# Performance work log

Measured on AMD Instinct MI355X. Metric: run time of the kernel, lower is better.

Reference implementation:

```python
import jax, jax.numpy as jnp
import numpy as np

B, CIN, COUT = 4, 32, 32
D1, D2, D3 = 64, 64, 64
M1, M2, M3 = 32, 32, 17  # n_modes with last dim -> 32//2+1 after rfft redundancy
INIT_STD = (2.0 / (CIN + COUT)) ** 0.5


def setup_inputs() -> dict:
    key = jax.random.key(0)
    k_x, k_wr, k_wi, k_b = jax.random.split(key, 4)
    x = jax.random.normal(k_x, (B, CIN, D1, D2, D3), dtype=jnp.float32)
    # ComplexDense factorized weight, normal_(0, init_std) on real and imag parts
    w_real = INIT_STD * jax.random.normal(k_wr, (CIN, COUT, M1, M2, M3), dtype=jnp.float32)
    w_imag = INIT_STD * jax.random.normal(k_wi, (CIN, COUT, M1, M2, M3), dtype=jnp.float32)
    # bias: (n_layers=1, out_channels, 1, 1, 1); we take index 0 slice
    bias = INIT_STD * jax.random.normal(k_b, (1, COUT, 1, 1, 1), dtype=jnp.float32)
    return {"x": x, "w_real": w_real, "w_imag": w_imag, "bias": bias}


def reference(x, w_real, w_imag, bias):
    fft_axes = (-3, -2, -1)
    b, cin, d1, d2, d3 = x.shape
    f3 = d3 // 2 + 1
    # forward rFFT, shift all but last (real) axis so low modes are centered
    xf = jnp.fft.rfftn(x, axes=fft_axes)               # (B, Cin, D1, D2, f3) complex
    xf = jnp.fft.fftshift(xf, axes=fft_axes[:-1])
    weight = w_real + 1j * w_imag                       # (Cin, Cout, M1, M2, M3)
    m1, m2, m3 = weight.shape[2:]
    s1, s2 = (d1 - m1) // 2, (d2 - m2) // 2
    xs = xf[:, :, s1:s1 + m1, s2:s2 + m2, :m3]          # centered low modes
    # channel contraction in Fourier space: abcde,bfcde->afcde
    out_modes = jnp.einsum('abcde,bfcde->afcde', xs, weight)
    out_fft = jnp.zeros((b, weight.shape[1], d1, d2, f3), dtype=out_modes.dtype)
    out_fft = out_fft.at[:, :, s1:s1 + m1, s2:s2 + m2, :m3].set(out_modes)
    # torch applies fftshift (not ifftshift); identical for even sizes
    out_fft = jnp.fft.fftshift(out_fft, axes=fft_axes[:-1])
    out = jnp.fft.irfftn(out_fft, s=(d1, d2, d3), axes=fft_axes)
    return out + bias[0]
```

## Files before the change

### kernel.cpp

```cpp
#include <hip/hip_runtime.h>
#include <math.h>

static constexpr int NB  = 4;
static constexpr int NC  = 32;

__device__ __attribute__((aligned(256))) float T3F[64 * 48];
__device__ __attribute__((aligned(256))) float2 T3I2[17 * 64];
__device__ __attribute__((aligned(256))) float T12F[64 * 64];
__device__ __attribute__((aligned(256))) float TINV[32 * 128];

__global__ __launch_bounds__(256) void k0_init() {
    const int t = blockIdx.x * 256 + threadIdx.x;
    if (t < 64 * 17) {
        int n = t / 17, k = t % 17;
        int idx = (n * k) & 63;
        float s, c;
        sincospif(idx / 32.0f, &s, &c);
        T3F[n * 48 + 2 * k] = c;  T3F[n * 48 + 2 * k + 1] = -s;
    }
    if (t < 64) {
        for (int q = 34; q < 48; ++q) T3F[t * 48 + q] = 0.f;
    }
    if (t < 17 * 64) {
        int k = t >> 6, n = t & 63;
        int idx = (n * k) & 63;
        float s, c;
        sincospif(idx / 32.0f, &s, &c);
        T3I2[t] = make_float2(c, s);
    }
    if (t < 64 * 32) {
        int n = t / 32, p = t % 32;
        int o = (p + 48) & 63;
        int idx = (o * n) & 63;
        float s, c;
        sincospif(idx / 32.0f, &s, &c);
        T12F[n * 64 + 2 * p] = c;  T12F[n * 64 + 2 * p + 1] = -s;
    }
    if (t < 32 * 64) {
        int p = t / 64, n = t % 64;
        int o = (p + 48) & 63;
        int idx = (o * n) & 63;
        float s, c;
        sincospif(idx / 32.0f, &s, &c);
        TINV[p * 128 + 2 * n] = c;  TINV[p * 128 + 2 * n + 1] = s;
    }
}

__device__ __forceinline__ void cmadd(float2& a, float2 x, float wx, float wy) {
    a.x = fmaf(x.x, wx, fmaf(-x.y, wy, a.x));
    a.y = fmaf(x.x, wy, fmaf( x.y, wx, a.y));
}

__global__ __launch_bounds__(64)
void k1_rfft_d3(const float* __restrict__ x, float2* __restrict__ o1) {
    __shared__ float tile[64 * 65];
    const int t = threadIdx.x, bid = blockIdx.x;
    const float4* src4 = (const float4*)(x + (size_t)bid * 4096);
    for (int j = 0; j < 16; ++j) {
        int f4 = j * 64 + t;
        float4 v = src4[f4];
        int d2 = f4 >> 4, n0 = (f4 & 15) << 2;
        float* p = &tile[d2 * 65 + n0];
        p[0] = v.x; p[1] = v.y; p[2] = v.z; p[3] = v.w;
    }
    __syncthreads();
    float ar[17], ai[17];
#pragma unroll
    for (int k = 0; k < 17; ++k) { ar[k] = 0.f; ai[k] = 0.f; }
    const float* row = &tile[t * 65];
    for (int n = 0; n < 32; ++n) {
        float xa = row[n], xb = row[n + 32];
        float se = xa + xb, so = xa - xb;
        const float* w = &T3F[n * 48];
#pragma unroll
        for (int k = 0; k < 17; ++k) {
            float xv = (k & 1) ? so : se;
            ar[k] = fmaf(xv, w[2 * k], ar[k]);
            ai[k] = fmaf(xv, w[2 * k + 1], ai[k]);
        }
    }
    const int bc = bid >> 6, d1 = bid & 63;
    float2* dst = o1 + (size_t)bc * (17 * 4096) + d1 * 64 + t;
#pragma unroll
    for (int k = 0; k < 17; ++k)
        dst[(size_t)k * 4096] = make_float2(ar[k], ai[k]);
}

__global__ __launch_bounds__(256)
void k2a_dft_d2(const float2* __restrict__ in, float2* __restrict__ T) {
    __shared__ float smem[8320];
    float* re = smem;
    float* im = smem + 64 * 65;
    const int t = threadIdx.x;
    const size_t base = (size_t)blockIdx.x * 4096;
    for (int j = 0; j < 16; ++j) {
        int idx = j * 256 + t;
        float2 v = in[base + idx];
        int d1 = idx >> 6, n2 = idx & 63;
        re[d1 * 65 + n2] = v.x;
        im[d1 * 65 + n2] = v.y;
    }
    __syncthreads();
    const int d1 = t & 63;
    const int pg = __builtin_amdgcn_readfirstlane(t >> 6);
    float2 acc[8];
#pragma unroll
    for (int j = 0; j < 8; ++j) acc[j] = make_float2(0.f, 0.f);
    const float* rrow = &re[d1 * 65];
    const float* irow = &im[d1 * 65];
#pragma unroll 2
    for (int n2 = 0; n2 < 64; ++n2) {
        float xr = rrow[n2], xi = irow[n2];
        const float* w = &T12F[n2 * 64 + pg * 16];
#pragma unroll
        for (int j = 0; j < 8; ++j)
            cmadd(acc[j], make_float2(xr, xi), w[2 * j], w[2 * j + 1]);
    }
    __syncthreads();
    float2* tile = (float2*)smem;
#pragma unroll
    for (int j = 0; j < 8; ++j) tile[d1 * 33 + pg * 8 + j] = acc[j];
    __syncthreads();
    float2* dst = T + (size_t)blockIdx.x * 2048;
#pragma unroll
    for (int q = 0; q < 8; ++q) {
        int e = t * 8 + q;
        dst[e] = tile[(e >> 5) * 33 + (e & 31)];
    }
}

__global__ __launch_bounds__(544)
void k2b_dft_d1(const float2* __restrict__ T, float2* __restrict__ Y) {
    __shared__ float2 tile[8 * 544];
    const int u = threadIdx.x;
    const int bc = blockIdx.x, pg = blockIdx.y;
    const int k3 = u >> 5, p2 = u & 31;
    const float2* src = T + ((size_t)bc * 17 + k3) * 2048 + p2;
    float2 acc[8];
#pragma unroll
    for (int j = 0; j < 8; ++j) acc[j] = make_float2(0.f, 0.f);
#pragma unroll 2
    for (int n1 = 0; n1 < 64; ++n1) {
        float2 xv = src[n1 * 32];
        const float* w = &T12F[n1 * 64 + pg * 16];
#pragma unroll
        for (int j = 0; j < 8; ++j)
            cmadd(acc[j], xv, w[2 * j], w[2 * j + 1]);
    }
#pragma unroll
    for (int j = 0; j < 8; ++j)
        tile[j * 544 + p2 * 17 + k3] = acc[j];
    __syncthreads();
    float2* dst = Y + (size_t)bc * 17408 + (size_t)pg * 8 * 544;
#pragma unroll
    for (int i = 0; i < 8; ++i)
        dst[u + i * 544] = tile[u + i * 544];
}

__global__ __launch_bounds__(64)
void k3_mix(const float2* __restrict__ Y, const float* __restrict__ wr,
            const float* __restrict__ wi, float2* __restrict__ Z) {
    const int m = blockIdx.x * 64 + threadIdx.x;
    const int ch = blockIdx.y;
    float2 acc[4][2];
#pragma unroll
    for (int a = 0; a < 4; ++a)
#pragma unroll
        for (int co = 0; co < 2; ++co) acc[a][co] = make_float2(0.f, 0.f);
#pragma unroll 8
    for (int cin = 0; cin < 32; ++cin) {
        float2 xv[4];
#pragma unroll
        for (int a = 0; a < 4; ++a)
            xv[a] = Y[((size_t)a * 32 + cin) * 17408 + m];
        size_t wb = ((size_t)cin * 32 + ch * 2) * 17408 + m;
#pragma unroll
        for (int co = 0; co < 2; ++co) {
            float wrv = wr[wb + (size_t)co * 17408];
            float wiv = wi[wb + (size_t)co * 17408];
#pragma unroll
            for (int a = 0; a < 4; ++a)
                cmadd(acc[a][co], xv[a], wrv, wiv);
        }
    }
#pragma unroll
    for (int a = 0; a < 4; ++a)
#pragma unroll
        for (int co = 0; co < 2; ++co)
            Z[((size_t)a * 32 + ch * 2 + co) * 17408 + m] = acc[a][co];
}

__global__ __launch_bounds__(544)
void k4a_idft_d1(const float2* __restrict__ Z, float2* __restrict__ U) {
    const int u = threadIdx.x;
    const int bf = blockIdx.x, ng = blockIdx.y;
    const float2* src = Z + (size_t)bf * 17408 + u;
    float2 acc[8];
#pragma unroll
    for (int j = 0; j < 8; ++j) acc[j] = make_float2(0.f, 0.f);
#pragma unroll 2
    for (int p1 = 0; p1 < 32; ++p1) {
        float2 xv = src[(size_t)p1 * 544];
        const float* w = &TINV[p1 * 128 + ng * 16];
#pragma unroll
        for (int j = 0; j < 8; ++j)
            cmadd(acc[j], xv, w[2 * j], w[2 * j + 1]);
    }
    float2* dst = U + (size_t)bf * 34816 + (size_t)ng * 8 * 544 + u;
#pragma unroll
    for (int j = 0; j < 8; ++j) dst[(size_t)j * 544] = acc[j];
}

__global__ __launch_bounds__(256)
void k45_ifft23(const float2* __restrict__ U, const float* __restrict__ bias,
                float* __restrict__ out) {
    __shared__ __align__(16) float2 Ur[32 * 18];
    __shared__ float2 W2[17 * 64];
    const int t = threadIdx.x;
    const int bf = blockIdx.x, n1 = blockIdx.y;
    const float2* src = U + (size_t)bf * 34816 + (size_t)n1 * 544;
    for (int j = t; j < 544; j += 256) {
        int p2 = j / 17, k3 = j - p2 * 17;
        Ur[p2 * 18 + k3] = src[j];
    }
    const int lane = t & 63;
    const int w = __builtin_amdgcn_readfirstlane(t >> 6);
    float2 tws[32];
#pragma unroll
    for (int p = 0; p < 32; ++p)
        tws[p] = *(const float2*)&TINV[p * 128 + 2 * lane];
    __syncthreads();
    const float inv2 = 2.0f / 262144.0f;
    {
        const int kb = w * 4;
        float A[4] = {0,0,0,0}, Bm[4] = {0,0,0,0};
        float C[4] = {0,0,0,0}, Dm[4] = {0,0,0,0};
#pragma unroll
        for (int p2 = 0; p2 < 32; ++p2) {
            float4 xa = *(const float4*)&Ur[p2 * 18 + kb];
            float4 xb = *(const float4*)&Ur[p2 * 18 + kb + 2];
            float c = tws[p2].x, s = tws[p2].y;
            A[0] = fmaf(xa.x, c, A[0]);  Bm[0] = fmaf(xa.y, s, Bm[0]);
            C[0] = fmaf(xa.x, s, C[0]);  Dm[0] = fmaf(xa.y, c, Dm[0]);
            A[1] = fmaf(xa.z, c, A[1]);  Bm[1] = fmaf(xa.w, s, Bm[1]);
            C[1] = fmaf(xa.z, s, C[1]);  Dm[1] = fmaf(xa.w, c, Dm[1]);
            A[2] = fmaf(xb.x, c, A[2]);  Bm[2] = fmaf(xb.y, s, Bm[2]);
            C[2] = fmaf(xb.x, s, C[2]);  Dm[2] = fmaf(xb.y, c, Dm[2]);
            A[3] = fmaf(xb.z, c, A[3]);  Bm[3] = fmaf(xb.w, s, Bm[3]);
            C[3] = fmaf(xb.z, s, C[3]);  Dm[3] = fmaf(xb.w, c, Dm[3]);
        }
#pragma unroll
        for (int j = 0; j < 4; ++j)
            W2[(kb + j) * 64 + lane] =
                make_float2((A[j] - Bm[j]) * inv2, (C[j] + Dm[j]) * inv2);
        if (w == 3) {
            float a = 0.f, b = 0.f, c2 = 0.f, d = 0.f;
#pragma unroll
            for (int p2 = 0; p2 < 32; ++p2) {
                float2 xv = Ur[p2 * 18 + 16];
                float c = tws[p2].x, s = tws[p2].y;
                a  = fmaf(xv.x, c, a);   b = fmaf(xv.y, s, b);
                c2 = fmaf(xv.x, s, c2);  d = fmaf(xv.y, c, d);
            }
            W2[16 * 64 + lane] = make_float2((a - b) * inv2, (c2 + d) * inv2);
        }
    }
    __syncthreads();
    float2 X[17];
#pragma unroll
    for (int k = 0; k < 17; ++k) X[k] = W2[k * 64 + lane];
    const float bv = bias[bf & 31];
    float y[16];
#pragma unroll
    for (int r = 0; r < 16; ++r) y[r] = fmaf(X[0].x, 0.5f, bv);
#pragma unroll
    for (int k = 1; k < 17; ++k) {
        const float2* tr = &T3I2[k * 64 + w * 16];
#pragma unroll
        for (int r = 0; r < 16; ++r) {
            float2 tw = tr[r];
            y[r] = fmaf(X[k].x, tw.x, y[r]);
            y[r] = fmaf(-X[k].y, tw.y, y[r]);
        }
    }
    float* dst = out + (size_t)bf * 262144 + (size_t)n1 * 4096
               + (size_t)lane * 64 + w * 16;
#pragma unroll
    for (int q = 0; q < 4; ++q)
        *(float4*)&dst[q * 4] =
            make_float4(y[q * 4], y[q * 4 + 1], y[q * 4 + 2], y[q * 4 + 3]);
}

extern "C" void kernel_launch(void* const* d_in, const int* in_sizes, int n_in,
                              void* d_out, int out_size, void* d_ws, size_t ws_size,
                              hipStream_t stream) {
    const float* x    = (const float*)d_in[0];
    const float* wr   = (const float*)d_in[1];
    const float* wi   = (const float*)d_in[2];
    const float* bias = (const float*)d_in[3];
    float* out = (float*)d_out;

    float2* A = (float2*)d_ws;
    float2* B = A + (size_t)2176 * 4096;
    float2* Y = A;
    float2* Z = A + (size_t)17825792 / 8;

    k0_init    <<<8, 256, 0, stream>>>();
    k1_rfft_d3 <<<NB * NC * 64, 64, 0, stream>>>(x, A);
    k2a_dft_d2 <<<2176, 256, 0, stream>>>(A, B);
    k2b_dft_d1 <<<dim3(128, 4), 544, 0, stream>>>(B, Y);
    k3_mix     <<<dim3(272, 16), 64, 0, stream>>>(Y, wr, wi, Z);
    k4a_idft_d1<<<dim3(128, 8), 544, 0, stream>>>(Z, B);
    k45_ifft23 <<<dim3(128, 64), 256, 0, stream>>>(B, bias, out);
}
```

Before: 276.9 us.

## Fuse d3 rFFT with d2 DFT in one kernel using even/odd split

Measured after the change: 247.6 us. -10.6%, faster.

```diff
diff --git a/kernel.cpp b/kernel.cpp
--- a/kernel.cpp
+++ b/kernel.cpp
@@ -52,8 +52,11 @@
 }
 
 __global__ __launch_bounds__(64)
-void k1_rfft_d3(const float* __restrict__ x, float2* __restrict__ o1) {
-    __shared__ float tile[64 * 65];
+void k12_rfft_dft(const float* __restrict__ x, float2* __restrict__ T) {
+    __shared__ __align__(16) float smem[64 * 65];
+    float* tile = smem;
+    float2* XE = (float2*)smem;
+    float2* XO = XE + 17 * 33;
     const int t = threadIdx.x, bid = blockIdx.x;
     const float4* src4 = (const float4*)(x + (size_t)bid * 4096);
     for (int j = 0; j < 16; ++j) {
@@ -63,7 +66,6 @@
         float* p = &tile[d2 * 65 + n0];
         p[0] = v.x; p[1] = v.y; p[2] = v.z; p[3] = v.w;
     }
-    __syncthreads();
     float ar[17], ai[17];
 #pragma unroll
     for (int k = 0; k < 17; ++k) { ar[k] = 0.f; ai[k] = 0.f; }
@@ -79,53 +81,34 @@
             ai[k] = fmaf(xv, w[2 * k + 1], ai[k]);
         }
     }
+    const int lane = t;
+    const int nl = lane & 31;
+#pragma unroll
+    for (int k = 0; k < 17; ++k) {
+        float pr = __shfl_xor(ar[k], 32);
+        float pi = __shfl_xor(ai[k], 32);
+        if (lane < 32) XE[k * 33 + nl] = make_float2(ar[k] + pr, ai[k] + pi);
+        else           XO[k * 33 + nl] = make_float2(pr - ar[k], pi - ai[k]);
+    }
+    const int p2 = lane & 31;
+    const int kh = lane >> 5;
+    float2 twv[32];
+#pragma unroll
+    for (int n = 0; n < 32; ++n)
+        twv[n] = *(const float2*)&T12F[n * 64 + 2 * p2];
+    const float2* Xs = (p2 & 1) ? XO : XE;
     const int bc = bid >> 6, d1 = bid & 63;
-    float2* dst = o1 + (size_t)bc * (17 * 4096) + d1 * 64 + t;
-#pragma unroll
-    for (int k = 0; k < 17; ++k)
-        dst[(size_t)k * 4096] = make_float2(ar[k], ai[k]);
-}
-
-__global__ __launch_bounds__(256)
-void k2a_dft_d2(const float2* __restrict__ in, float2* __restrict__ T) {
-    __shared__ float smem[8320];
-    float* re = smem;
-    float* im = smem + 64 * 65;
-    const int t = threadIdx.x;
-    const size_t base = (size_t)blockIdx.x * 4096;
-    for (int j = 0; j < 16; ++j) {
-        int idx = j * 256 + t;
-        float2 v = in[base + idx];
-        int d1 = idx >> 6, n2 = idx & 63;
-        re[d1 * 65 + n2] = v.x;
-        im[d1 * 65 + n2] = v.y;
-    }
-    __syncthreads();
-    const int d1 = t & 63;
-    const int pg = __builtin_amdgcn_readfirstlane(t >> 6);
-    float2 acc[8];
-#pragma unroll
-    for (int j = 0; j < 8; ++j) acc[j] = make_float2(0.f, 0.f);
-    const float* rrow = &re[d1 * 65];
-    const float* irow = &im[d1 * 65];
-#pragma unroll 2
-    for (int n2 = 0; n2 < 64; ++n2) {
-        float xr = rrow[n2], xi = irow[n2];
-        const float* w = &T12F[n2 * 64 + pg * 16];
-#pragma unroll
-        for (int j = 0; j < 8; ++j)
-            cmadd(acc[j], make_float2(xr, xi), w[2 * j], w[2 * j + 1]);
-    }
-    __syncthreads();
-    float2* tile = (float2*)smem;
-#pragma unroll
-    for (int j = 0; j < 8; ++j) tile[d1 * 33 + pg * 8 + j] = acc[j];
-    __syncthreads();
-    float2* dst = T + (size_t)blockIdx.x * 2048;
-#pragma unroll
-    for (int q = 0; q < 8; ++q) {
-        int e = t * 8 + q;
-        dst[e] = tile[(e >> 5) * 33 + (e & 31)];
+#pragma unroll
+    for (int j = 0; j < 9; ++j) {
+        int k3 = kh * 9 + j;
+        if (k3 < 17) {
+            float2 s = make_float2(0.f, 0.f);
+            const float2* xr = &Xs[k3 * 33];
+#pragma unroll
+            for (int n2 = 0; n2 < 32; ++n2)
+                cmadd(s, xr[n2], twv[n2].x, twv[n2].y);
+            T[((size_t)bc * 17 + k3) * 2048 + d1 * 32 + p2] = s;
+        }
     }
 }
 
@@ -305,11 +288,10 @@
     float2* Y = A;
     float2* Z = A + (size_t)17825792 / 8;
 
-    k0_init    <<<8, 256, 0, stream>>>();
-    k1_rfft_d3 <<<NB * NC * 64, 64, 0, stream>>>(x, A);
-    k2a_dft_d2 <<<2176, 256, 0, stream>>>(A, B);
-    k2b_dft_d1 <<<dim3(128, 4), 544, 0, stream>>>(B, Y);
-    k3_mix     <<<dim3(272, 16), 64, 0, stream>>>(Y, wr, wi, Z);
-    k4a_idft_d1<<<dim3(128, 8), 544, 0, stream>>>(Z, B);
-    k45_ifft23 <<<dim3(128, 64), 256, 0, stream>>>(B, bias, out);
-}
+    k0_init     <<<8, 256, 0, stream>>>();
+    k12_rfft_dft<<<NB * NC * 64, 64, 0, stream>>>(x, B);
+    k2b_dft_d1  <<<dim3(128, 4), 544, 0, stream>>>(B, Y);
+    k3_mix      <<<dim3(272, 16), 64, 0, stream>>>(Y, wr, wi, Z);
+    k4a_idft_d1 <<<dim3(128, 8), 544, 0, stream>>>(Z, B);
+    k45_ifft23  <<<dim3(128, 64), 256, 0, stream>>>(B, bias, out);
+}
```
